# Optimization experiments

Measured on AMD Instinct MI355X. Metric: run time of the kernel, lower is better.

Reference implementation:

```python
import jax, jax.numpy as jnp
import numpy as np

KSIZE = 11
EPS = 1e-6

def _gauss_kernel(k=KSIZE, sigma=None):
    if sigma is None:
        sigma = k
    p = k // 2
    coords = np.arange(k) - p
    yy, xx = np.meshgrid(coords, coords, indexing='ij')
    g = np.exp(-(xx ** 2 + yy ** 2) / (2.0 * sigma ** 2))
    g = g / g.sum()
    return jnp.asarray(g, dtype=jnp.float32)

def setup_inputs() -> dict:
    key = jax.random.key(0)
    k1, k2 = jax.random.split(key)
    B, C, H, W = 16, 64, 256, 256
    x = jax.random.normal(k1, (B, C, H, W), dtype=jnp.float32)
    y = jax.random.normal(k2, (B, C, H, W), dtype=jnp.float32)
    gauss = _gauss_kernel()
    return {"x": x, "y": y, "gauss": gauss}

def reference(x, y, gauss):
    # Fused form: weighted local sums of x^2, y^2, x*y are SAME-padded
    # cross-correlations of the channel-summed products with the Gaussian.
    # This matches torch Unfold(padding=K//2) zero-padding semantics exactly.
    B, C, H, W = x.shape
    # channel-reduced local statistics inputs: [3, B, H, W]
    s = jnp.stack([
        jnp.sum(x * x, axis=1),
        jnp.sum(x * y, axis=1),
        jnp.sum(y * y, axis=1),
    ], axis=0)
    inp = s.reshape(3 * B, 1, H, W)              # NCHW
    ker = gauss[None, None, :, :]                # OIHW (symmetric -> corr==conv)
    out = jax.lax.conv_general_dilated(
        inp, ker, window_strides=(1, 1), padding='SAME',
        dimension_numbers=('NCHW', 'OIHW', 'NCHW'))
    xx, xy, yy = out.reshape(3, B, H, W)
    x_norm = jnp.sqrt(xx)
    y_norm = jnp.sqrt(yy)
    return xy / (x_norm * y_norm + EPS)
```

## Files before the change

kernel.cpp:

```cpp
#include <hip/hip_runtime.h>
#include <math.h>

constexpr int B = 16, C = 64, H = 256, W = 256;
constexpr int HW = H * W;
constexpr int BHW = B * HW;
constexpr int K = 11, P = 5;
#define EPS 1e-6f

__global__ __launch_bounds__(256) void k_reduce(
    const float* __restrict__ x, const float* __restrict__ y,
    float* __restrict__ s )
{
    const int GPI = HW / 4;
    int idx = blockIdx.x * 256 + threadIdx.x;
    int b = idx >> 14;
    int g = idx & (GPI - 1);

    const float4* x4 = (const float4*)x + (size_t)b * C * GPI + g;
    const float4* y4 = (const float4*)y + (size_t)b * C * GPI + g;

    float4 axx = make_float4(0.f, 0.f, 0.f, 0.f);
    float4 axy = axx, ayy = axx;

#pragma unroll 8
    for (int c = 0; c < C; ++c) {
        float4 xv = x4[c * GPI];
        float4 yv = y4[c * GPI];
        axx.x += xv.x * xv.x; axx.y += xv.y * xv.y;
        axx.z += xv.z * xv.z; axx.w += xv.w * xv.w;
        axy.x += xv.x * yv.x; axy.y += xv.y * yv.y;
        axy.z += xv.z * yv.z; axy.w += xv.w * yv.w;
        ayy.x += yv.x * yv.x; ayy.y += yv.y * yv.y;
        ayy.z += yv.z * yv.z; ayy.w += yv.w * yv.w;
    }

    float4* s4 = (float4*)s;
    int o = idx;
    s4[o]                 = axx;
    s4[(BHW / 4) + o]     = axy;
    s4[2 * (BHW / 4) + o] = ayy;
}


__global__ __launch_bounds__(256) void k_hblur(
    const float* __restrict__ s, const float* __restrict__ gauss,
    float* __restrict__ t )
{
    int idx = blockIdx.x * 256 + threadIdx.x;
    int w = idx & (W - 1);
    int rowbase = idx - w;

    float inv = 1.0f / sqrtf(gauss[5 * K + 5]);
    float wt[K];
#pragma unroll
    for (int j = 0; j < K; ++j) wt[j] = gauss[5 * K + j] * inv;

    float a0 = 0.f, a1 = 0.f, a2 = 0.f;
#pragma unroll
    for (int j = 0; j < K; ++j) {
        int ww = w + j - P;
        if (ww < 0 || ww >= W) continue;
        float wj = wt[j];
        a0 += wj * s[rowbase + ww];
        a1 += wj * s[BHW + rowbase + ww];
        a2 += wj * s[2 * BHW + rowbase + ww];
    }
    t[idx]           = a0;
    t[BHW + idx]     = a1;
    t[2 * BHW + idx] = a2;
}

__global__ __launch_bounds__(256) void k_vblur_combine(
    const float* __restrict__ t, const float* __restrict__ gauss,
    float* __restrict__ out )
{
    int idx = blockIdx.x * 256 + threadIdx.x;
    int hw = idx & (HW - 1);
    int h = hw >> 8;

    float inv = 1.0f / sqrtf(gauss[5 * K + 5]);
    float wt[K];
#pragma unroll
    for (int i = 0; i < K; ++i) wt[i] = gauss[i * K + 5] * inv;

    float axx = 0.f, axy = 0.f, ayy = 0.f;
#pragma unroll
    for (int i = 0; i < K; ++i) {
        int hh = h + i - P;
        if (hh < 0 || hh >= H) continue;
        float wi = wt[i];
        int off = idx + (i - P) * W;
        axx += wi * t[off];
        axy += wi * t[BHW + off];
        ayy += wi * t[2 * BHW + off];
    }
    out[idx] = axy / (sqrtf(axx) * sqrtf(ayy) + EPS);
}

extern "C" void kernel_launch(void* const* d_in, const int* in_sizes, int n_in,
                              void* d_out, int out_size, void* d_ws, size_t ws_size,
                              hipStream_t stream) {
    const float* x     = (const float*)d_in[0];
    const float* y     = (const float*)d_in[1];
    const float* gauss = (const float*)d_in[2];
    float* out = (float*)d_out;

    float* s = (float*)d_ws;
    float* t = s + 3 * BHW;

    k_reduce<<<B * (HW / 4) / 256, 256, 0, stream>>>(x, y, s);
    k_hblur<<<BHW / 256, 256, 0, stream>>>(s, gauss, t);
    k_vblur_combine<<<BHW / 256, 256, 0, stream>>>(t, gauss, out);
}
```

Before: 539.0 us.

## Fuse horizontal and vertical blur into tiled LDS kernel; split channel reduction

Merges the separate horizontal and vertical blur kernels into one kernel. It loads a 32x32 tile plus halo of the three statistic maps into shared memory, blurs both directions there and writes the final ratio, so the intermediate buffer never goes through global memory. The reduce kernel now splits the 64 channels between two thread halves and combines them through LDS, which doubles the number of blocks for more memory parallelism. The cost is halo overhead, LDS pressure that may reduce occupancy, and an extra sync in the reduce kernel.

After: 528.7 us. About the same (-1.9%).

```diff
diff --git a/kernel.cpp b/kernel.cpp
--- a/kernel.cpp
+++ b/kernel.cpp
@@ -12,18 +12,23 @@
     float* __restrict__ s )
 {
     const int GPI = HW / 4;
-    int idx = blockIdx.x * 256 + threadIdx.x;
-    int b = idx >> 14;
-    int g = idx & (GPI - 1);
+    __shared__ float4 lds[3][128];
 
-    const float4* x4 = (const float4*)x + (size_t)b * C * GPI + g;
-    const float4* y4 = (const float4*)y + (size_t)b * C * GPI + g;
+    int t = threadIdx.x;
+    int half = t >> 7;
+    int lane = t & 127;
+    int gidx = blockIdx.x * 128 + lane;
+    int b = gidx >> 14;
+    int g = gidx & (GPI - 1);
+
+    const float4* x4 = (const float4*)x + ((size_t)b * C + half * 32) * GPI + g;
+    const float4* y4 = (const float4*)y + ((size_t)b * C + half * 32) * GPI + g;
 
     float4 axx = make_float4(0.f, 0.f, 0.f, 0.f);
     float4 axy = axx, ayy = axx;
 
 #pragma unroll 8
-    for (int c = 0; c < C; ++c) {
+    for (int c = 0; c < 32; ++c) {
         float4 xv = x4[c * GPI];
         float4 yv = y4[c * GPI];
         axx.x += xv.x * xv.x; axx.y += xv.y * xv.y;
@@ -34,67 +39,92 @@
         ayy.z += yv.z * yv.z; ayy.w += yv.w * yv.w;
     }
 
-    float4* s4 = (float4*)s;
-    int o = idx;
-    s4[o]                 = axx;
-    s4[(BHW / 4) + o]     = axy;
-    s4[2 * (BHW / 4) + o] = ayy;
+    if (half) {
+        lds[0][lane] = axx;
+        lds[1][lane] = axy;
+        lds[2][lane] = ayy;
+    }
+    __syncthreads();
+    if (!half) {
+        float4 bxx = lds[0][lane], bxy = lds[1][lane], byy = lds[2][lane];
+        axx.x += bxx.x; axx.y += bxx.y; axx.z += bxx.z; axx.w += bxx.w;
+        axy.x += bxy.x; axy.y += bxy.y; axy.z += bxy.z; axy.w += bxy.w;
+        ayy.x += byy.x; ayy.y += byy.y; ayy.z += byy.z; ayy.w += byy.w;
+
+        float4* s4 = (float4*)s;
+        s4[gidx]                  = axx;
+        s4[(BHW / 4) + gidx]      = axy;
+        s4[2 * (BHW / 4) + gidx]  = ayy;
+    }
 }
 
+constexpr int TH = 32, TW = 32;
+constexpr int RH = TH + K - 1;
+constexpr int RW = TW + K - 1;
+constexpr int RWP = RW + 2;
 
-__global__ __launch_bounds__(256) void k_hblur(
+__global__ __launch_bounds__(256) void k_blur_combine(
     const float* __restrict__ s, const float* __restrict__ gauss,
-    float* __restrict__ t )
+    float* __restrict__ out )
 {
-    int idx = blockIdx.x * 256 + threadIdx.x;
-    int w = idx & (W - 1);
-    int rowbase = idx - w;
+    __shared__ float raw[3][RH][RWP];
+    __shared__ float hb[3][RH][TW];
+
+    int t = threadIdx.x;
+    int blk = blockIdx.x;
+    int b  = blk >> 6;
+    int th = (blk >> 3) & 7;
+    int tw = blk & 7;
+    int h0 = th * TH, w0 = tw * TW;
 
     float inv = 1.0f / sqrtf(gauss[5 * K + 5]);
-    float wt[K];
+    float wr[K], wc[K];
 #pragma unroll
-    for (int j = 0; j < K; ++j) wt[j] = gauss[5 * K + j] * inv;
+    for (int j = 0; j < K; ++j) wr[j] = gauss[5 * K + j] * inv;
+#pragma unroll
+    for (int i = 0; i < K; ++i) wc[i] = gauss[i * K + 5] * inv;
 
-    float a0 = 0.f, a1 = 0.f, a2 = 0.f;
+    for (int m = 0; m < 3; ++m) {
+        const float* sp = s + m * BHW + b * HW;
+        for (int i = t; i < RH * RW; i += 256) {
+            int r = i / RW;
+            int c2 = i - r * RW;
+            int h = h0 - P + r;
+            int w = w0 - P + c2;
+            float v = 0.f;
+            if (h >= 0 && h < H && w >= 0 && w < W) v = sp[h * W + w];
+            raw[m][r][c2] = v;
+        }
+    }
+    __syncthreads();
+
+    for (int i = t; i < 3 * RH * TW; i += 256) {
+        int m = i / (RH * TW);
+        int rem = i - m * (RH * TW);
+        int r = rem >> 5;
+        int cc = rem & (TW - 1);
+        float a = 0.f;
 #pragma unroll
-    for (int j = 0; j < K; ++j) {
-        int ww = w + j - P;
-        if (ww < 0 || ww >= W) continue;
-        float wj = wt[j];
-        a0 += wj * s[rowbase + ww];
-        a1 += wj * s[BHW + rowbase + ww];
-        a2 += wj * s[2 * BHW + rowbase + ww];
+        for (int j = 0; j < K; ++j) a += wr[j] * raw[m][r][cc + j];
+        hb[m][r][cc] = a;
     }
-    t[idx]           = a0;
-    t[BHW + idx]     = a1;
-    t[2 * BHW + idx] = a2;
-}
+    __syncthreads();
 
-__global__ __launch_bounds__(256) void k_vblur_combine(
-    const float* __restrict__ t, const float* __restrict__ gauss,
-    float* __restrict__ out )
-{
-    int idx = blockIdx.x * 256 + threadIdx.x;
-    int hw = idx & (HW - 1);
-    int h = hw >> 8;
-
-    float inv = 1.0f / sqrtf(gauss[5 * K + 5]);
-    float wt[K];
 #pragma unroll
-    for (int i = 0; i < K; ++i) wt[i] = gauss[i * K + 5] * inv;
-
-    float axx = 0.f, axy = 0.f, ayy = 0.f;
+    for (int k = 0; k < 4; ++k) {
+        int idx = t + k * 256;
+        int rr = idx >> 5;
+        int cc = idx & (TW - 1);
+        float axx = 0.f, axy = 0.f, ayy = 0.f;
 #pragma unroll
-    for (int i = 0; i < K; ++i) {
-        int hh = h + i - P;
-        if (hh < 0 || hh >= H) continue;
-        float wi = wt[i];
-        int off = idx + (i - P) * W;
-        axx += wi * t[off];
-        axy += wi * t[BHW + off];
-        ayy += wi * t[2 * BHW + off];
+        for (int i = 0; i < K; ++i) {
+            float wi = wc[i];
+            axx += wi * hb[0][rr + i][cc];
+            axy += wi * hb[1][rr + i][cc];
+            ayy += wi * hb[2][rr + i][cc];
+        }
+        out[b * HW + (h0 + rr) * W + (w0 + cc)] = axy / (sqrtf(axx) * sqrtf(ayy) + EPS);
     }
-    out[idx] = axy / (sqrtf(axx) * sqrtf(ayy) + EPS);
 }
 
 extern "C" void kernel_launch(void* const* d_in, const int* in_sizes, int n_in,
@@ -106,9 +136,7 @@
     float* out = (float*)d_out;
 
     float* s = (float*)d_ws;
-    float* t = s + 3 * BHW;
 
-    k_reduce<<<B * (HW / 4) / 256, 256, 0, stream>>>(x, y, s);
-    k_hblur<<<BHW / 256, 256, 0, stream>>>(s, gauss, t);
-    k_vblur_combine<<<BHW / 256, 256, 0, stream>>>(t, gauss, out);
+    k_reduce<<<(B * (HW / 4)) / 128, 256, 0, stream>>>(x, y, s);
+    k_blur_combine<<<B * (H / TH) * (W / TW), 256, 0, stream>>>(s, gauss, out);
 }
```
